# Optimization experiments

Measured on AMD Instinct MI355X. Metric: run time of the kernel, lower is better.

Reference implementation:

```python
import jax, jax.numpy as jnp
from jax import lax
import numpy as np


def setup_inputs() -> dict:
    key = jax.random.key(0)
    ks = jax.random.split(key, 7)
    B, T, I, H, O = 8192, 512, 7, 7, 1
    s = 1.0 / np.sqrt(H)
    return {
        "x": jax.random.normal(ks[0], (B, T, I), dtype=jnp.float32),
        "W_ih": jax.random.normal(ks[1], (H, I), dtype=jnp.float32) * s,
        "W_hh": jax.random.normal(ks[2], (H, H), dtype=jnp.float32) * s,
        "b_ih": jax.random.normal(ks[3], (H,), dtype=jnp.float32) * s,
        "b_hh": jax.random.normal(ks[4], (H,), dtype=jnp.float32) * s,
        "W_fc": jax.random.normal(ks[5], (O, H), dtype=jnp.float32) * s,
        "b_fc": jax.random.normal(ks[6], (O,), dtype=jnp.float32) * s,
    }


def reference(x, W_ih, W_hh, b_ih, b_hh, W_fc, b_fc):
    # Vanilla tanh RNN: h_t = tanh(x_t W_ih^T + b_ih + h_{t-1} W_hh^T + b_hh)
    B, T, _ = x.shape
    H = W_hh.shape[0]
    # Precompute the input projection for all timesteps (one big GEMM).
    xp = jnp.einsum("bti,hi->bth", x, W_ih) + (b_ih + b_hh)  # [B,T,H]
    h0 = jnp.zeros((B, H), dtype=x.dtype)

    def step(h, xt):
        h = jnp.tanh(xt + h @ W_hh.T)
        return h, h

    hT, hs = lax.scan(step, h0, jnp.swapaxes(xp, 0, 1))  # hs: [T,B,H]
    out_seq = jnp.swapaxes(hs, 0, 1)  # [B,T,H]
    out = (jnp.einsum("bth,oh->bto", out_seq, W_fc) + b_fc).squeeze(-1)  # [B,T]
    hidden = hT[None]  # [1,B,H] matching torch's (num_layers, B, H)
    return (out, hidden)
```

## Files before the change

### kernel.cpp

```cpp
#include <hip/hip_runtime.h>
#include <stdint.h>


#define B_TOTAL 8192
#define T_STEPS 512

#define DPP_QUAD0 0x00
#define DPP_QUAD1 0x55
#define DPP_QUAD2 0xAA
#define DPP_QUAD3 0xFF
#define DPP_XOR1  0xB1
#define DPP_XOR2  0x4E
#define DPP_HM    0x141

template <int CTRL>
__device__ __forceinline__ float dpp_mov(float v) {
    int s = __float_as_int(v);
    return __int_as_float(__builtin_amdgcn_update_dpp(s, s, CTRL, 0xF, 0xF, true));
}

__device__ __forceinline__ float tanh_fast(float a) {
    float e = __builtin_amdgcn_exp2f(a * 2.8853900817779268f);
    float r = __builtin_amdgcn_rcpf(e + 1.0f);
    return __builtin_fmaf(-2.0f, r, 1.0f);
}

__global__ __launch_bounds__(512, 2) void rnn_kernel(
    const float* __restrict__ x,
    const float* __restrict__ Wih,
    const float* __restrict__ Whh,
    const float* __restrict__ bih,
    const float* __restrict__ bhh,
    const float* __restrict__ Wfc,
    const float* __restrict__ bfc,
    float* __restrict__ out)
{
    const int tid   = threadIdx.x;
    const int wid   = tid >> 6;
    const int role  = wid >> 2;
    const int pair  = wid & 3;
    const int lane  = tid & 63;
    const int k     = lane & 7;
    const int b     = blockIdx.x * 32 + pair * 8 + (lane >> 3);
    const int lbase = lane * 10;

    __shared__ __attribute__((aligned(16))) float lds_u[2][4][640];
    __shared__ __attribute__((aligned(16))) float lds_h[2][4][640];

    float wa[4] = {0.f, 0.f, 0.f, 0.f}, wb[4] = {0.f, 0.f, 0.f, 0.f};
    float ra0 = 0.f, ra1 = 0.f, ra2 = 0.f, ra3 = 0.f;
    float rb0 = 0.f, rb1 = 0.f, rb2 = 0.f, rb3 = 0.f;
    float wih[7] = {0.f, 0.f, 0.f, 0.f, 0.f, 0.f, 0.f};
    float bias = 0.f, wfc_own = 0.f, bfcv = 0.f;
    const float* xrow = x + (size_t)b * (T_STEPS * 7);
    float* outp = out + (size_t)b * T_STEPS;

    auto u_store = [&](const float4* xb, int par) {
        float xv[56];
        #pragma unroll
        for (int i = 0; i < 14; ++i) {
            xv[4 * i + 0] = xb[i].x; xv[4 * i + 1] = xb[i].y;
            xv[4 * i + 2] = xb[i].z; xv[4 * i + 3] = xb[i].w;
        }
        float u[8];
        #pragma unroll
        for (int s = 0; s < 8; ++s) {
            const float* xs = &xv[s * 7];
            float p01 = __builtin_fmaf(wih[1], xs[1], wih[0] * xs[0]);
            float p23 = __builtin_fmaf(wih[3], xs[3], wih[2] * xs[2]);
            float p45 = __builtin_fmaf(wih[5], xs[5], wih[4] * xs[4]);
            float p6b = __builtin_fmaf(wih[6], xs[6], bias);
            u[s] = (p01 + p23) + (p45 + p6b);
        }
        float2* up = (float2*)&lds_u[par][pair][lbase];
        up[0] = make_float2(u[0], u[1]);
        up[1] = make_float2(u[2], u[3]);
        up[2] = make_float2(u[4], u[5]);
        up[3] = make_float2(u[6], u[7]);
    };

    auto emit_out = [&](int t) {
        const float2* hp = (const float2*)&lds_h[t & 1][pair][lbase];
        float2 h01 = hp[0], h23 = hp[1], h45 = hp[2], h67 = hp[3];
        float hs[8] = {h01.x, h01.y, h23.x, h23.y, h45.x, h45.y, h67.x, h67.y};
        float o[8];
        #pragma unroll
        for (int s = 0; s < 8; ++s) {
            float v = wfc_own * hs[s];
            v += dpp_mov<DPP_XOR1>(v);
            v += dpp_mov<DPP_XOR2>(v);
            v += dpp_mov<DPP_HM>(v);
            o[s] = v + bfcv;
        }
        if (k == 7) {
            *(float4*)(outp + t * 8 + 0) = make_float4(o[0], o[1], o[2], o[3]);
            *(float4*)(outp + t * 8 + 4) = make_float4(o[4], o[5], o[6], o[7]);
        }
    };

    auto rec_step = [&](int par) {
        const float2* up = (const float2*)&lds_u[par][pair][lbase];
        float2 u01 = up[0], u23 = up[1], u45 = up[2], u67 = up[3];
        float u[8] = {u01.x, u01.y, u23.x, u23.y, u45.x, u45.y, u67.x, u67.y};
        float hs[8];
        #pragma unroll
        for (int s = 0; s < 8; ++s) {
            float p0 = __builtin_fmaf(wa[0], ra0, u[s]);
            float p1 = __builtin_fmaf(wa[2], ra2, wa[1] * ra1);
            float p2 = __builtin_fmaf(wb[0], rb0, wa[3] * ra3);
            float p3 = __builtin_fmaf(wb[2], rb2, wb[1] * rb1);
            float p4 = wb[3] * rb3;
            float acc = (p0 + p1) + (p2 + (p3 + p4));
            float hk = tanh_fast(acc);
            hs[s] = hk;
            ra0 = dpp_mov<DPP_QUAD0>(hk);
            ra1 = dpp_mov<DPP_QUAD1>(hk);
            ra2 = dpp_mov<DPP_QUAD2>(hk);
            ra3 = dpp_mov<DPP_QUAD3>(hk);
            rb0 = dpp_mov<DPP_HM>(ra0);
            rb1 = dpp_mov<DPP_HM>(ra1);
            rb2 = dpp_mov<DPP_HM>(ra2);
            rb3 = dpp_mov<DPP_HM>(ra3);
        }
        float2* hp = (float2*)&lds_h[par][pair][lbase];
        hp[0] = make_float2(hs[0], hs[1]);
        hp[1] = make_float2(hs[2], hs[3]);
        hp[2] = make_float2(hs[4], hs[5]);
        hp[3] = make_float2(hs[6], hs[7]);
    };

    if (role == 0) {
        const int quad = (lane >> 2) & 1;
        float whh_row[8];
        #pragma unroll
        for (int i = 0; i < 8; ++i) whh_row[i] = 0.0f;
        if (k < 7) {
            #pragma unroll
            for (int i = 0; i < 7; ++i) whh_row[i] = Whh[k * 7 + i];
        }
        #pragma unroll
        for (int j = 0; j < 4; ++j) {
            wa[j] = quad ? whh_row[4 + j] : whh_row[j];
            wb[j] = quad ? whh_row[j]     : whh_row[4 + j];
        }
    } else {
        if (k < 7) {
            #pragma unroll
            for (int i = 0; i < 7; ++i) wih[i] = Wih[k * 7 + i];
            bias = bih[k] + bhh[k];
            wfc_own = Wfc[k];
        }
        bfcv = bfc[0];
        float4 xb[14];
        const float4* src = (const float4*)xrow;
        #pragma unroll
        for (int i = 0; i < 14; ++i) xb[i] = src[i];
        u_store(xb, 0);
    }
    __syncthreads();

    #pragma unroll 1
    for (int t = 0; t < 64; ++t) {
        if (role == 0) {
            rec_step(t & 1);
        } else {
            float4 xb[14];
            if (t < 63) {
                const float4* src = (const float4*)(xrow + (t + 1) * 56);
                #pragma unroll
                for (int i = 0; i < 14; ++i) xb[i] = src[i];
            }
            if (t > 0) emit_out(t - 1);
            if (t < 63) u_store(xb, (t + 1) & 1);
        }
        __syncthreads();
    }

    if (role == 0) {
        if (k < 7) {
            int kk = k & 3;
            float hv = (kk == 0) ? ra0 : (kk == 1) ? ra1 : (kk == 2) ? ra2 : ra3;
            out[(size_t)B_TOTAL * T_STEPS + (size_t)b * 7 + k] = hv;
        }
    } else {
        emit_out(63);
    }
}

extern "C" void kernel_launch(void* const* d_in, const int* in_sizes, int n_in,
                              void* d_out, int out_size, void* d_ws, size_t ws_size,
                              hipStream_t stream) {
    const float* x   = (const float*)d_in[0];
    const float* Wih = (const float*)d_in[1];
    const float* Whh = (const float*)d_in[2];
    const float* bih = (const float*)d_in[3];
    const float* bhh = (const float*)d_in[4];
    const float* Wfc = (const float*)d_in[5];
    const float* bfc = (const float*)d_in[6];
    float* out = (float*)d_out;

    rnn_kernel<<<dim3(B_TOTAL / 32), dim3(512), 0, stream>>>(
        x, Wih, Whh, bih, bhh, Wfc, bfc, out);
}
```

Measured before the change: 240.9 us.

## Shrink blocks to one recurrence/producer wave pair and prefetch x two chunks ahead

Each block shrinks from 4 wave pairs (512 threads, 32 batch rows) to a single recurrence wave plus a single producer wave (128 threads, 8 rows), with 4x as many blocks. The goal is to make each __syncthreads cover only two waves, so the recurrence wave no longer waits on the slowest of eight. The producer now keeps the next x chunk in registers and issues the load for the chunk after that before the barrier, hiding global load latency for a full step. The cost is more blocks and launch-level scheduling, plus extra registers for the prefetch buffer, which may lower occupancy.

```diff
diff --git a/kernel.cpp b/kernel.cpp
--- a/kernel.cpp
+++ b/kernel.cpp
@@ -25,7 +25,7 @@
     return __builtin_fmaf(-2.0f, r, 1.0f);
 }
 
-__global__ __launch_bounds__(512, 2) void rnn_kernel(
+__global__ __launch_bounds__(128, 2) void rnn_kernel(
     const float* __restrict__ x,
     const float* __restrict__ Wih,
     const float* __restrict__ Whh,
@@ -36,16 +36,14 @@
     float* __restrict__ out)
 {
     const int tid   = threadIdx.x;
-    const int wid   = tid >> 6;
-    const int role  = wid >> 2;
-    const int pair  = wid & 3;
+    const int role  = tid >> 6;
     const int lane  = tid & 63;
     const int k     = lane & 7;
-    const int b     = blockIdx.x * 32 + pair * 8 + (lane >> 3);
+    const int b     = blockIdx.x * 8 + (lane >> 3);
     const int lbase = lane * 10;
 
-    __shared__ __attribute__((aligned(16))) float lds_u[2][4][640];
-    __shared__ __attribute__((aligned(16))) float lds_h[2][4][640];
+    __shared__ __attribute__((aligned(16))) float lds_u[2][640];
+    __shared__ __attribute__((aligned(16))) float lds_h[2][640];
 
     float wa[4] = {0.f, 0.f, 0.f, 0.f}, wb[4] = {0.f, 0.f, 0.f, 0.f};
     float ra0 = 0.f, ra1 = 0.f, ra2 = 0.f, ra3 = 0.f;
@@ -54,6 +52,7 @@
     float bias = 0.f, wfc_own = 0.f, bfcv = 0.f;
     const float* xrow = x + (size_t)b * (T_STEPS * 7);
     float* outp = out + (size_t)b * T_STEPS;
+    float4 xa[14];
 
     auto u_store = [&](const float4* xb, int par) {
         float xv[56];
@@ -72,7 +71,7 @@
             float p6b = __builtin_fmaf(wih[6], xs[6], bias);
             u[s] = (p01 + p23) + (p45 + p6b);
         }
-        float2* up = (float2*)&lds_u[par][pair][lbase];
+        float2* up = (float2*)&lds_u[par][lbase];
         up[0] = make_float2(u[0], u[1]);
         up[1] = make_float2(u[2], u[3]);
         up[2] = make_float2(u[4], u[5]);
@@ -80,7 +79,7 @@
     };
 
     auto emit_out = [&](int t) {
-        const float2* hp = (const float2*)&lds_h[t & 1][pair][lbase];
+        const float2* hp = (const float2*)&lds_h[t & 1][lbase];
         float2 h01 = hp[0], h23 = hp[1], h45 = hp[2], h67 = hp[3];
         float hs[8] = {h01.x, h01.y, h23.x, h23.y, h45.x, h45.y, h67.x, h67.y};
         float o[8];
@@ -99,7 +98,7 @@
     };
 
     auto rec_step = [&](int par) {
-        const float2* up = (const float2*)&lds_u[par][pair][lbase];
+        const float2* up = (const float2*)&lds_u[par][lbase];
         float2 u01 = up[0], u23 = up[1], u45 = up[2], u67 = up[3];
         float u[8] = {u01.x, u01.y, u23.x, u23.y, u45.x, u45.y, u67.x, u67.y};
         float hs[8];
@@ -122,7 +121,7 @@
             rb2 = dpp_mov<DPP_HM>(ra2);
             rb3 = dpp_mov<DPP_HM>(ra3);
         }
-        float2* hp = (float2*)&lds_h[par][pair][lbase];
+        float2* hp = (float2*)&lds_h[par][lbase];
         hp[0] = make_float2(hs[0], hs[1]);
         hp[1] = make_float2(hs[2], hs[3]);
         hp[2] = make_float2(hs[4], hs[5]);
@@ -151,11 +150,14 @@
             wfc_own = Wfc[k];
         }
         bfcv = bfc[0];
-        float4 xb[14];
-        const float4* src = (const float4*)xrow;
-        #pragma unroll
-        for (int i = 0; i < 14; ++i) xb[i] = src[i];
-        u_store(xb, 0);
+        float4 x0[14];
+        const float4* s0 = (const float4*)xrow;
+        #pragma unroll
+        for (int i = 0; i < 14; ++i) x0[i] = s0[i];
+        u_store(x0, 0);
+        const float4* s1 = (const float4*)(xrow + 56);
+        #pragma unroll
+        for (int i = 0; i < 14; ++i) xa[i] = s1[i];
     }
     __syncthreads();
 
@@ -164,14 +166,14 @@
         if (role == 0) {
             rec_step(t & 1);
         } else {
-            float4 xb[14];
             if (t < 63) {
-                const float4* src = (const float4*)(xrow + (t + 1) * 56);
+                u_store(xa, (t + 1) & 1);
+                const int nc = (t + 2 <= 63) ? (t + 2) : 0;
+                const float4* src = (const float4*)(xrow + nc * 56);
                 #pragma unroll
-                for (int i = 0; i < 14; ++i) xb[i] = src[i];
+                for (int i = 0; i < 14; ++i) xa[i] = src[i];
             }
             if (t > 0) emit_out(t - 1);
-            if (t < 63) u_store(xb, (t + 1) & 1);
         }
         __syncthreads();
     }
@@ -199,6 +201,6 @@
     const float* bfc = (const float*)d_in[6];
     float* out = (float*)d_out;
 
-    rnn_kernel<<<dim3(B_TOTAL / 32), dim3(512), 0, stream>>>(
+    rnn_kernel<<<dim3(B_TOTAL / 8), dim3(128), 0, stream>>>(
         x, Wih, Whh, bih, bhh, Wfc, bfc, out);
 }
```

Result: faster. 230.7 us (-4.2%).
